# Performance work log

Hardware: AMD Instinct MI355X
Metric: run time of the kernel (lower is better)

The kernel has to match this reference:

```python
import jax, jax.numpy as jnp
import numpy as np
from jax.scipy.linalg import expm

B, Q, F, R, T, H = 2048, 16, 512, 400, 50, 256
STEPS = 100
DT = 1.0 / STEPS
COH = 50.0  # coherence_time


def setup_inputs() -> dict:
    ks = jax.random.split(jax.random.key(0), 48)
    it = iter(range(48))
    def rn(shape, s=1.0):
        return jax.random.normal(ks[next(it)], shape, dtype=jnp.float32) * s
    A = rn((Q, Q)); Bm = rn((Q, Q))
    d = {
        'molecular_features': rn((B, F)),
        'noise': rn((B, T, R), 0.1),          # torch.randn_like * 0.1
        'amp_re': rn((B, Q)), 'amp_im': rn((B, Q)),
        'H_re': (A + A.T) / 2.0,               # hermitized: real part symmetric
        'H_im': (Bm - Bm.T) / 2.0,             # imag part antisymmetric
        'gpc': rn((R,)),
        'bw1': rn((256, Q + F), (Q + F) ** -0.5), 'bb1': rn((256,), 0.01),
        'bw2': rn((128, 256), 256 ** -0.5), 'bb2': rn((128,), 0.01),
        'bw3': rn((R, 128), 128 ** -0.5), 'bb3': rn((R,), 0.01),
    }
    ins = [R, H, H]
    for l in range(3):
        d[f'Wih{l}'] = rn((4 * H, ins[l]), ins[l] ** -0.5)
        d[f'Whh{l}'] = rn((4 * H, H), H ** -0.5)
        d[f'bih{l}'] = rn((4 * H,), 0.01)
        d[f'bhh{l}'] = rn((4 * H,), 0.01)
    d.update({
        'cw1': rn((512, H + R), (H + R) ** -0.5), 'cb1': rn((512,), 0.01),
        'cw2': rn((256, 512), 512 ** -0.5), 'cb2': rn((256,), 0.01),
        'cw3': rn((64, 256), 256 ** -0.5), 'cb3': rn((64,), 0.01),
        'cw4': rn((1, 64), 64 ** -0.5), 'cb4': rn((1,), 0.01),
    })
    return d


def _lstm_layer(x, Wih, Whh, bih, bhh):
    # PyTorch LSTM gate order: i, f, g, o
    def step(carry, xt):
        h, c = carry
        z = xt @ Wih.T + h @ Whh.T + bih + bhh
        ig, fg, gg, og = jnp.split(z, 4, axis=-1)
        c = jax.nn.sigmoid(fg) * c + jax.nn.sigmoid(ig) * jnp.tanh(gg)
        h = jax.nn.sigmoid(og) * jnp.tanh(c)
        return (h, c), h
    n = x.shape[0]
    init = (jnp.zeros((n, H), x.dtype), jnp.zeros((n, H), x.dtype))
    (hT, _), hs = jax.lax.scan(step, init, jnp.swapaxes(x, 0, 1))
    return jnp.swapaxes(hs, 0, 1), hT


def _forward(molecular_features, noise, amp_re, amp_im, H_re, H_im, gpc,
             bw1, bb1, bw2, bb2, bw3, bb3,
             Wih0, Whh0, bih0, bhh0, Wih1, Whh1, bih1, bhh1, Wih2, Whh2, bih2, bhh2,
             cw1, cb1, cw2, cb2, cw3, cb3, cw4, cb4):
    Hp = (H_re + 1j * H_im).astype(jnp.complex64)
    amp = (amp_re + 1j * amp_im).astype(jnp.complex64)
    amp = amp / jnp.linalg.norm(amp, axis=-1, keepdims=True)  # F.normalize
    # molecular interaction Hamiltonian (real part only, as in source)
    M = jnp.einsum('bi,ij->bij', molecular_features[:, :Q], H_re)
    def qstep(a, step):
        t = step * DT
        Ht = Hp[None, :, :] + M * t                 # [B,Q,Q] complex
        U = jax.vmap(expm)(-1j * Ht * DT)           # per-sample matrix_exp
        a = jnp.einsum('bij,bj->bi', U, a) * jnp.exp(-t / COH)
        return a, None
    amp, _ = jax.lax.scan(qstep, amp, jnp.arange(STEPS, dtype=jnp.float32))
    obs = (jnp.abs(amp) ** 2).astype(jnp.float32)   # quantum observables
    bio = jnp.concatenate([obs, molecular_features], axis=-1)  # [B, Q+F]
    h1 = jax.nn.relu(bio @ bw1.T + bb1)
    h2 = jnp.tanh(h1 @ bw2.T + bb2)
    receptor = jax.nn.sigmoid(h2 @ bw3.T + bb3)     # [B, R]
    # biological signal transduction
    g_amp = receptor * jax.nn.sigmoid(gpc)
    adapt = jnp.exp(-jnp.arange(T, dtype=jnp.float32) / 10.0)[None, :, None]
    seq = g_amp[:, None, :] * adapt + noise         # [B, T, R]
    x, hT = _lstm_layer(seq, Wih0, Whh0, bih0, bhh0)
    x, hT = _lstm_layer(x, Wih1, Whh1, bih1, bhh1)
    x, hT = _lstm_layer(x, Wih2, Whh2, bih2, bhh2)  # hT: last-layer hidden [B,H]
    cf = jnp.concatenate([hT, receptor], axis=-1)   # [B, H+R]
    c1 = jax.nn.relu(cf @ cw1.T + cb1)
    c2 = jax.nn.relu(c1 @ cw2.T + cb2)
    c3 = jnp.tanh(c2 @ cw3.T + cb3)
    cons = jnp.mean(jax.nn.sigmoid(c3 @ cw4.T + cb4))
    valence = jnp.mean(jnp.tanh(x), axis=(1, 2))    # [B]
    return receptor, x, valence, cons, amp


def reference(molecular_features, noise, amp_re, amp_im, H_re, H_im, gpc,
              bw1, bb1, bw2, bb2, bw3, bb3,
              Wih0, Whh0, bih0, bhh0, Wih1, Whh1, bih1, bhh1, Wih2, Whh2, bih2, bhh2,
              cw1, cb1, cw2, cb2, cw3, cb3, cw4, cb4):
    receptor, seq, valence, cons, amp = _forward(
        molecular_features, noise, amp_re, amp_im, H_re, H_im, gpc,
        bw1, bb1, bw2, bb2, bw3, bb3,
        Wih0, Whh0, bih0, bhh0, Wih1, Whh1, bih1, bhh1, Wih2, Whh2, bih2, bhh2,
        cw1, cb1, cw2, cb2, cw3, cb3, cw4, cb4)
    # von Neumann entanglement entropy across a 2/2 qubit bipartition (Q=16 -> 4x4)
    half = 2 ** ((int(np.log2(Q))) // 2)
    rs = amp.reshape(amp.shape[0], half, -1)
    rho = jnp.einsum('bij,bik->bjk', rs, jnp.conj(rs))
    ev = jnp.clip(jnp.linalg.eigvals(rho).real, 1e-12, None)
    ent = jnp.mean(-jnp.sum(ev * jnp.log(ev), axis=-1))
    return receptor, seq, valence, cons, ent
```

## Files before the change

### kernel.cpp

```cpp
#include <hip/hip_runtime.h>
#include <stdint.h>


using short8 = __attribute__((ext_vector_type(8))) short;
using f32x4  = __attribute__((ext_vector_type(4))) float;

#define DEV static __device__ __forceinline__

typedef const __attribute__((address_space(1))) void GV;
typedef __attribute__((address_space(3))) void LV;
DEV void gload16(const void* g, void* l) {
  __builtin_amdgcn_global_load_lds((GV*)g, (LV*)l, 16, 0, 0);
}

DEV ushort f2b(float x) {
  union { float f; uint32_t u; } v; v.f = x;
  uint32_t r = v.u + 0x7FFFu + ((v.u >> 16) & 1u);
  return (ushort)(r >> 16);
}
DEV float b2f(ushort x) {
  union { uint32_t u; float f; } v; v.u = ((uint32_t)x) << 16; return v.f;
}
DEV float sigf(float x) { return 1.f / (1.f + __expf(-x)); }
DEV float tanh_fast(float x) {
  float xc = fminf(9.f, fmaxf(-9.f, x));
  float e = __expf(2.f * xc);
  return (e - 1.f) / (e + 1.f);
}

__global__ void k_convw(const float* __restrict__ src, ushort* __restrict__ dst,
                        int sr, int dr, int sc, int dc,
                        const float* __restrict__ scale, int mode) {
  long n = (long)dr * dc;
  for (long idx = (long)blockIdx.x * blockDim.x + threadIdx.x; idx < n;
       idx += (long)gridDim.x * blockDim.x) {
    int r = (int)(idx / dc), c = (int)(idx % dc);
    float v = 0.f;
    if (r < sr && c < sc) {
      v = src[(long)r * sc + c];
      if (mode == 1) v *= sigf(scale[c]);
    }
    dst[idx] = f2b(v);
  }
}

__global__ void k_vadd(const float* __restrict__ a, const float* __restrict__ b,
                       float* __restrict__ o, int n) {
  int i = blockIdx.x * blockDim.x + threadIdx.x;
  if (i < n) o[i] = a[i] + b[i];
}

__global__ __launch_bounds__(128)
void k_quantum(const float* __restrict__ ampr_in, const float* __restrict__ ampi_in,
               const float* __restrict__ Hre, const float* __restrict__ Him,
               const float* __restrict__ mf,
               ushort* __restrict__ bio, float* __restrict__ ampS_r,
               float* __restrict__ ampS_i, int st0) {
  const int gid = blockIdx.x * 128 + threadIdx.x;
  const int b = gid >> 5;
  const int l32 = gid & 31;
  const int i = l32 & 15;
  const int h = l32 >> 4;
  float hre[8], him[8];
#pragma unroll
  for (int jj = 0; jj < 8; jj++) {
    hre[jj] = Hre[i * 16 + h * 8 + jj];
    him[jj] = Him[i * 16 + h * 8 + jj];
  }
  const float mfi = mf[(long)b * 512 + i];
  float are, aim;
  if (st0 == 0) {
    are = ampr_in[b * 16 + i]; aim = ampi_in[b * 16 + i];
    float ss = are * are + aim * aim;
#pragma unroll
    for (int m = 1; m < 32; m <<= 1) ss += __shfl_xor(ss, m, 32);
    ss *= 0.5f;
    const float inv = 1.f / sqrtf(ss);
    are *= inv; aim *= inv;
  } else {
    are = ampS_r[b * 16 + i]; aim = ampS_i[b * 16 + i];
  }
#pragma unroll 1
  for (int st = st0; st < st0 + 25; ++st) {
    const float t = (float)st * 0.01f;
    const float fac = 1.f + t * mfi;
    const float dec = __expf(-t * 0.02f);
    float tre = are, tim = aim, rre = are, rim = aim;
#pragma unroll 1
    for (int k = 1; k <= 6; k++) {
      float w1r = 0.f, w1i = 0.f, w2r = 0.f, w2i = 0.f;
#pragma unroll
      for (int jj = 0; jj < 8; jj++) {
        const float vr = __shfl(tre, h * 8 + jj, 32);
        const float vi = __shfl(tim, h * 8 + jj, 32);
        w1r += hre[jj] * vr; w1i += hre[jj] * vi;
        w2r += him[jj] * vr; w2i += him[jj] * vi;
      }
      w1r += __shfl_xor(w1r, 16, 32);
      w1i += __shfl_xor(w1i, 16, 32);
      w2r += __shfl_xor(w2r, 16, 32);
      w2i += __shfl_xor(w2i, 16, 32);
      const float hr = w1r * fac - w2i;
      const float hi = w1i * fac + w2r;
      const float sk = 0.01f / (float)k;
      tre = sk * hi; tim = -sk * hr;
      rre += tre; rim += tim;
    }
    are = rre * dec; aim = rim * dec;
  }
  if (h == 0) {
    ampS_r[b * 16 + i] = are;
    ampS_i[b * 16 + i] = aim;
    if (bio) bio[(long)b * 576 + i] = f2b(are * are + aim * aim);
  }
}

__global__ void k_biofill(const float* __restrict__ mf, ushort* __restrict__ bio) {
  long i = (long)blockIdx.x * blockDim.x + threadIdx.x;
  if (i < (long)2048 * 512) {
    long b = i >> 9, k = i & 511;
    bio[b * 576 + 16 + k] = f2b(mf[i]);
  }
}

template<int BT>
__global__ __launch_bounds__(256)
void k_gemm(const ushort* __restrict__ A, int lda,
            const ushort* __restrict__ W, int ldw,
            const float* __restrict__ bias,
            const ushort* __restrict__ Gg, int t0,
            float* __restrict__ Cf, int ldcf,
            ushort* __restrict__ Cb, int ldcb,
            int N, int K, int act, int swz) {
  constexpr int FR = BT / 32;
  constexpr int CH = BT / 32;
  __shared__ __align__(16) ushort lsA[2][BT * 64];
  __shared__ __align__(16) ushort lsB[2][BT * 64];
  const int tid = threadIdx.x;
  const int lane = tid & 63, w = tid >> 6;
  const int lr = lane & 15, lq = lane >> 4;
  const int wm = (w >> 1) * (BT / 2), wn = (w & 1) * (BT / 2);
  int bxb = blockIdx.x, byb = blockIdx.y;
  if (swz) {
    const int id = byb * gridDim.x + bxb;
    const int xcd = id & 7, q = id >> 3;
    byb = (q >> 4) * 16 + xcd * 2 + (q & 1);
    bxb = (q >> 1) & 7;
  }
  const int bm = byb * BT, bn = bxb * BT;
  const int srow = lane >> 3;
  const int scol = (((lane & 7) ^ srow)) * 8;

  auto stage = [&](int buf, int kk) {
#pragma unroll
    for (int c = 0; c < CH; c++) {
      const int ch = w * CH + c;
      const int r = ch * 8 + srow;
      gload16(A + (size_t)(bm + r) * lda + kk + scol, lsA[buf] + ch * 512);
      gload16(W + (size_t)(bn + r) * ldw + kk + scol, lsB[buf] + ch * 512);
    }
  };

  f32x4 acc[FR][FR];
#pragma unroll
  for (int i = 0; i < FR; i++)
#pragma unroll
    for (int j = 0; j < FR; j++) acc[i][j] = (f32x4){0.f, 0.f, 0.f, 0.f};

  stage(0, 0);
  __syncthreads();
  const int T = K >> 6;
  for (int t = 0; t < T; t++) {
    const int cur = t & 1;
    if (t + 1 < T) stage(cur ^ 1, (t + 1) * 64);
    short8 af[FR][2], bf[FR][2];
#pragma unroll
    for (int mi = 0; mi < FR; mi++)
#pragma unroll
      for (int k2 = 0; k2 < 2; k2++) {
        const int row = wm + mi * 16 + lr;
        af[mi][k2] = *(const short8*)(lsA[cur] + (row >> 3) * 512 + (row & 7) * 64 +
                                      (((k2 * 4 + lq) ^ (row & 7)) * 8));
      }
#pragma unroll
    for (int ni = 0; ni < FR; ni++)
#pragma unroll
      for (int k2 = 0; k2 < 2; k2++) {
        const int row = wn + ni * 16 + lr;
        bf[ni][k2] = *(const short8*)(lsB[cur] + (row >> 3) * 512 + (row & 7) * 64 +
                                      (((k2 * 4 + lq) ^ (row & 7)) * 8));
      }
#pragma unroll
    for (int k2 = 0; k2 < 2; k2++)
#pragma unroll
      for (int mi = 0; mi < FR; mi++)
#pragma unroll
        for (int ni = 0; ni < FR; ni++)
          acc[mi][ni] = __builtin_amdgcn_mfma_f32_16x16x32_bf16(
              af[mi][k2], bf[ni][k2], acc[mi][ni], 0, 0, 0);
    __syncthreads();
  }

#pragma unroll
  for (int mi = 0; mi < FR; mi++) {
#pragma unroll
    for (int r = 0; r < 4; r++) {
      const int row = bm + wm + mi * 16 + lq * 4 + r;
      float gfac = 0.f; const ushort* ggrow = nullptr;
      if (Gg) {
        gfac = __expf(-(float)(t0 + (row >> 11)) * 0.1f);
        ggrow = Gg + (size_t)(row & 2047) * 1024;
      }
#pragma unroll
      for (int ni = 0; ni < FR; ni++) {
        const int col = bn + wn + ni * 16 + lr;
        if (col < N) {
          float v = acc[mi][ni][r];
          if (bias) v += bias[col];
          if (Gg)  v += gfac * b2f(ggrow[col]);
          if (act == 1) v = fmaxf(v, 0.f);
          else if (act == 2) v = tanh_fast(v);
          else if (act == 3) v = sigf(v);
          if (Cf) Cf[(size_t)row * ldcf + col] = v;
          if (Cb) Cb[(size_t)row * ldcb + col] = f2b(v);
        }
      }
    }
  }
}

__global__ void k_noiseconv(const float* __restrict__ noise, ushort* __restrict__ dst, int t0) {
  long n = 10L * 2048 * 448;
  for (long idx = (long)blockIdx.x * blockDim.x + threadIdx.x; idx < n;
       idx += (long)gridDim.x * blockDim.x) {
    int r = (int)(idx % 448);
    long row = idx / 448;
    int b = (int)(row & 2047);
    int tl = (int)(row >> 11);
    ushort v = 0;
    if (r < 400)
      v = f2b(__builtin_nontemporal_load(&noise[((long)b * 50 + t0 + tl) * 400 + r]));
    dst[idx] = v;
  }
}

__global__ __launch_bounds__(512, 2)
void k_fused(const ushort* __restrict__ IH, const ushort* __restrict__ Whh,
             float* __restrict__ hstate, float* __restrict__ cstate,
             ushort* __restrict__ Hout, float* __restrict__ Xout, int t0,
             const ushort* __restrict__ gA, int glda,
             const ushort* __restrict__ gW,
             const float* __restrict__ gbias, const ushort* __restrict__ gGg,
             int gt0, ushort* __restrict__ gC, int gK) {
  __shared__ __align__(16) ushort upool[37024];
  const int tid = threadIdx.x;

  if (blockIdx.x < 128) {
    ushort (*h_lds)[266] = (ushort(*)[266])upool;
    ushort* ih0 = upool + 4256;
    const int lane = tid & 63, w8 = tid >> 6;
    const int lr = lane & 15, lq = lane >> 4;
    const int b0 = blockIdx.x * 16;
    const int wcols = w8 * 32;

    short8 wres[2][8];
#pragma unroll
    for (int cg = 0; cg < 2; cg++) {
      const ushort* wp = Whh + (size_t)(wcols + cg * 16 + lr) * 256 + lq * 8;
#pragma unroll
      for (int kk = 0; kk < 8; kk++) wres[cg][kk] = *(const short8*)(wp + kk * 32);
    }

    float c_reg[2][4], h_reg[2][4];
#pragma unroll
    for (int cg = 0; cg < 2; cg++) {
      const int j = wcols + cg * 16 + lr;
#pragma unroll
      for (int r = 0; r < 4; r++) {
        const int s = lq * 4 + r;
        float hv = hstate[(size_t)(b0 + s) * 256 + j];
        c_reg[cg][r] = cstate[(size_t)(b0 + s) * 256 + j];
        h_reg[cg][r] = hv;
        h_lds[s][j] = f2b(hv);
      }
    }
    __syncthreads();

#define LOADB(buf, g, cg) { \
  const ushort* wp_ = Whh + (size_t)((g) * 256 + wcols + (cg) * 16 + lr) * 256 + lq * 8; \
  _Pragma("unroll") for (int kk = 0; kk < 8; kk++) (buf)[kk] = *(const short8*)(wp_ + kk * 32); }
#define MFMAB(buf, g, cg) { \
  _Pragma("unroll") for (int kk = 0; kk < 8; kk++) \
    acc[cg][g] = __builtin_amdgcn_mfma_f32_16x16x32_bf16(af[kk], (buf)[kk], acc[cg][g], 0, 0, 0); }
#define MFMAR(cg) { \
  _Pragma("unroll") for (int kk = 0; kk < 8; kk++) \
    acc[cg][0] = __builtin_amdgcn_mfma_f32_16x16x32_bf16(af[kk], wres[cg][kk], acc[cg][0], 0, 0, 0); }

    for (int blk = 0; blk < 10; blk += 2) {
#pragma unroll
      for (int si = 0; si < 2; si++) {
        const ushort* src = IH + ((size_t)(blk + si) * 2048 + b0) * 1024;
#pragma unroll
        for (int u = 0; u < 4; u++) {
          const int bi = u * 8 + w8;
          gload16(src + (size_t)bi * 512 + lane * 8, ih0 + si * 16384 + bi * 512);
        }
      }
      __syncthreads();

      for (int i2 = 0; i2 < 2; i2++) {
        const int tl = blk + i2;
        const ushort* ihc = ih0 + i2 * 16384;
        short8 af[8];
#pragma unroll
        for (int kk = 0; kk < 8; kk++)
          af[kk] = *(const short8*)(&h_lds[lr][kk * 32 + lq * 8]);
        __syncthreads();

        f32x4 acc[2][4];
#pragma unroll
        for (int cg = 0; cg < 2; cg++)
#pragma unroll
          for (int g = 0; g < 4; g++) acc[cg][g] = (f32x4){0.f, 0.f, 0.f, 0.f};

        short8 wb0[8], wb1[8];
        LOADB(wb0, 1, 0);
        LOADB(wb1, 1, 1);
        MFMAR(0);
        MFMAR(1);
        MFMAB(wb0, 1, 0);
        LOADB(wb0, 2, 0);
        MFMAB(wb1, 1, 1);
        LOADB(wb1, 2, 1);
        MFMAB(wb0, 2, 0);
        LOADB(wb0, 3, 0);
        MFMAB(wb1, 2, 1);
        LOADB(wb1, 3, 1);
        MFMAB(wb0, 3, 0);
        MFMAB(wb1, 3, 1);

        const int t = t0 + tl;
#pragma unroll
        for (int cg = 0; cg < 2; cg++) {
          const int j = wcols + cg * 16 + lr;
#pragma unroll
          for (int r = 0; r < 4; r++) {
            const int s = lq * 4 + r;
            const float zi = acc[cg][0][r] + b2f(ihc[s * 1024 + j]);
            const float zf = acc[cg][1][r] + b2f(ihc[s * 1024 + 256 + j]);
            const float zg = acc[cg][2][r] + b2f(ihc[s * 1024 + 512 + j]);
            const float zo = acc[cg][3][r] + b2f(ihc[s * 1024 + 768 + j]);
            const float ig = sigf(zi), fg = sigf(zf), gg = tanh_fast(zg), og = sigf(zo);
            const float c = fg * c_reg[cg][r] + ig * gg;
            c_reg[cg][r] = c;
            const float h = og * tanh_fast(c);
            h_reg[cg][r] = h;
            h_lds[s][j] = f2b(h);
            if (Hout) Hout[((size_t)t * 2048 + b0 + s) * 256 + j] = f2b(h);
            if (Xout)
              __builtin_nontemporal_store(h, &Xout[((size_t)(b0 + s) * 50 + t) * 256 + j]);
          }
        }
        __syncthreads();
      }
    }
#undef LOADB
#undef MFMAB
#undef MFMAR
#pragma unroll
    for (int cg = 0; cg < 2; cg++) {
      const int j = wcols + cg * 16 + lr;
#pragma unroll
      for (int r = 0; r < 4; r++) {
        const int s = lq * 4 + r;
        hstate[(size_t)(b0 + s) * 256 + j] = h_reg[cg][r];
        cstate[(size_t)(b0 + s) * 256 + j] = c_reg[cg][r];
      }
    }
  } else {
    ushort* lsA = upool;
    ushort* lsB = upool + 16384;
    const int gb = blockIdx.x - 128;
    const int xcd = gb & 7, q = gb >> 3;
    const int byb = (q >> 4) * 16 + xcd * 2 + (q & 1);
    const int bxb = (q >> 1) & 7;
    const int bm = byb * 128, bn = bxb * 128;
    const int lane = tid & 63, w4 = tid >> 6;
    const int lr = lane & 15, lq = lane >> 4;
    const int wm = (w4 >> 1) * 64, wn = (w4 & 1) * 64;
    const int srow = lane >> 3;
    const int scol = (((lane & 7) ^ srow)) * 8;
    const bool gact = (tid < 256);

    f32x4 acc[4][4];
#pragma unroll
    for (int i = 0; i < 4; i++)
#pragma unroll
      for (int j = 0; j < 4; j++) acc[i][j] = (f32x4){0.f, 0.f, 0.f, 0.f};

    if (gact) {
#pragma unroll
      for (int c = 0; c < 4; c++) {
        const int ch = w4 * 4 + c;
        const int r = ch * 8 + srow;
        gload16(gA + (size_t)(bm + r) * glda + scol, lsA + ch * 512);
        gload16(gW + (size_t)(bn + r) * glda + scol, lsB + ch * 512);
      }
    }
    __syncthreads();

    const int T = gK >> 6;
    for (int t = 0; t < T; t++) {
      const int cur = t & 1;
      if (gact && t + 1 < T) {
        const int kk = (t + 1) * 64;
#pragma unroll
        for (int c = 0; c < 4; c++) {
          const int ch = w4 * 4 + c;
          const int r = ch * 8 + srow;
          gload16(gA + (size_t)(bm + r) * glda + kk + scol, lsA + (cur ^ 1) * 8192 + ch * 512);
          gload16(gW + (size_t)(bn + r) * glda + kk + scol, lsB + (cur ^ 1) * 8192 + ch * 512);
        }
      }
      if (gact) {
        short8 af[4][2], bf[4][2];
#pragma unroll
        for (int mi = 0; mi < 4; mi++)
#pragma unroll
          for (int k2 = 0; k2 < 2; k2++) {
            const int row = wm + mi * 16 + lr;
            af[mi][k2] = *(const short8*)(lsA + cur * 8192 + (row >> 3) * 512 +
                                          (row & 7) * 64 + (((k2 * 4 + lq) ^ (row & 7)) * 8));
          }
#pragma unroll
        for (int ni = 0; ni < 4; ni++)
#pragma unroll
          for (int k2 = 0; k2 < 2; k2++) {
            const int row = wn + ni * 16 + lr;
            bf[ni][k2] = *(const short8*)(lsB + cur * 8192 + (row >> 3) * 512 +
                                          (row & 7) * 64 + (((k2 * 4 + lq) ^ (row & 7)) * 8));
          }
#pragma unroll
        for (int k2 = 0; k2 < 2; k2++)
#pragma unroll
          for (int mi = 0; mi < 4; mi++)
#pragma unroll
            for (int ni = 0; ni < 4; ni++)
              acc[mi][ni] = __builtin_amdgcn_mfma_f32_16x16x32_bf16(
                  af[mi][k2], bf[ni][k2], acc[mi][ni], 0, 0, 0);
      }
      __syncthreads();
    }

    if (gact) {
#pragma unroll
      for (int mi = 0; mi < 4; mi++) {
#pragma unroll
        for (int r = 0; r < 4; r++) {
          const int row = bm + wm + mi * 16 + lq * 4 + r;
          float gfac = 0.f; const ushort* ggrow = nullptr;
          if (gGg) {
            gfac = __expf(-(float)(gt0 + (row >> 11)) * 0.1f);
            ggrow = gGg + (size_t)(row & 2047) * 1024;
          }
#pragma unroll
          for (int ni = 0; ni < 4; ni++) {
            const int col = bn + wn + ni * 16 + lr;
            float v = acc[mi][ni][r];
            if (gbias) v += gbias[col];
            if (gGg)  v += gfac * b2f(ggrow[col]);
            gC[(size_t)row * 1024 + col] = f2b(v);
          }
        }
      }
    }
  }
}

__global__ void k_cffill(const float* __restrict__ hT, const ushort* __restrict__ recb,
                         ushort* __restrict__ cf) {
  long i = (long)blockIdx.x * blockDim.x + threadIdx.x;
  if (i < (long)2048 * 656) {
    long b = i / 656; int c = (int)(i % 656);
    cf[b * 704 + c] = (c < 256) ? f2b(hT[b * 256 + c]) : recb[b * 448 + (c - 256)];
  }
}

__global__ __launch_bounds__(256)
void k_cons(const float* __restrict__ c3, const float* __restrict__ w4,
            const float* __restrict__ b4, float* __restrict__ out) {
  __shared__ float red[256];
  float accv = 0.f;
  for (int b = threadIdx.x; b < 2048; b += 256) {
    float d = b4[0];
#pragma unroll
    for (int k = 0; k < 64; k++) d += c3[(long)b * 64 + k] * w4[k];
    accv += sigf(d);
  }
  red[threadIdx.x] = accv; __syncthreads();
  for (int s = 128; s > 0; s >>= 1) {
    if (threadIdx.x < s) red[threadIdx.x] += red[threadIdx.x + s];
    __syncthreads();
  }
  if (threadIdx.x == 0) out[0] = red[0] * (1.f / 2048.f);
}

__global__ __launch_bounds__(256)
void k_val(const float* __restrict__ x, float* __restrict__ out) {
  __shared__ float red[256];
  const float* p = x + (size_t)blockIdx.x * 12800;
  float a = 0.f;
  for (int i = threadIdx.x; i < 12800; i += 256) a += tanh_fast(p[i]);
  red[threadIdx.x] = a; __syncthreads();
  for (int s = 128; s > 0; s >>= 1) {
    if (threadIdx.x < s) red[threadIdx.x] += red[threadIdx.x + s];
    __syncthreads();
  }
  if (threadIdx.x == 0) out[blockIdx.x] = red[0] * (1.f / 12800.f);
}

__global__ __launch_bounds__(64)
void k_ent(const float* __restrict__ ar, const float* __restrict__ ai,
           float* __restrict__ partial) {
  __shared__ float red[64];
  const int tid = threadIdx.x;
  const int b = blockIdx.x * 64 + tid;
  float vr[16], vi[16];
#pragma unroll
  for (int i = 0; i < 16; i++) { vr[i] = ar[b * 16 + i]; vi[i] = ai[b * 16 + i]; }
  float m[64];
#pragma unroll
  for (int j = 0; j < 4; j++)
#pragma unroll
    for (int k = 0; k < 4; k++) {
      float re = 0.f, im = 0.f;
#pragma unroll
      for (int i = 0; i < 4; i++) {
        float xr = vr[i * 4 + j], xi = vi[i * 4 + j];
        float yr = vr[i * 4 + k], yi = vi[i * 4 + k];
        re += xr * yr + xi * yi;
        im += xi * yr - xr * yi;
      }
      m[j * 8 + k] = re;
      m[j * 8 + (k + 4)] = -im;
      m[(j + 4) * 8 + k] = im;
      m[(j + 4) * 8 + (k + 4)] = re;
    }
#pragma unroll 1
  for (int sweep = 0; sweep < 6; ++sweep) {
#pragma unroll
    for (int p = 0; p < 7; p++) {
#pragma unroll
      for (int q = p + 1; q < 8; q++) {
        const float apq = m[p * 8 + q];
        if (fabsf(apq) > 1e-28f) {
          const float app = m[p * 8 + p], aqq = m[q * 8 + q];
          const float tau = (aqq - app) / (2.f * apq);
          const float tt = (tau >= 0.f ? 1.f : -1.f) /
                           (fabsf(tau) + sqrtf(1.f + tau * tau));
          const float cc = 1.f / sqrtf(1.f + tt * tt);
          const float ssn = tt * cc;
#pragma unroll
          for (int k2 = 0; k2 < 8; k2++) {
            const float mp = m[p * 8 + k2], mq = m[q * 8 + k2];
            m[p * 8 + k2] = cc * mp - ssn * mq;
            m[q * 8 + k2] = ssn * mp + cc * mq;
          }
#pragma unroll
          for (int k2 = 0; k2 < 8; k2++) {
            const float mp = m[k2 * 8 + p], mq = m[k2 * 8 + q];
            m[k2 * 8 + p] = cc * mp - ssn * mq;
            m[k2 * 8 + q] = ssn * mp + cc * mq;
          }
        }
      }
    }
  }
  float e = 0.f;
#pragma unroll
  for (int k2 = 0; k2 < 8; k2++) {
    const float lam = fmaxf(m[k2 * 8 + k2], 1e-12f);
    e -= lam * logf(lam);
  }
  red[tid] = e; __syncthreads();
  for (int s = 32; s > 0; s >>= 1) {
    if (tid < s) red[tid] += red[tid + s];
    __syncthreads();
  }
  if (tid == 0) partial[blockIdx.x] = red[0];
}

__global__ void k_entfin(const float* __restrict__ partial, float* __restrict__ out) {
  if (threadIdx.x == 0) {
    float s = 0.f;
    for (int i = 0; i < 32; i++) s += partial[i];
    out[0] = s * (0.5f / 2048.f);
  }
}

extern "C" void kernel_launch(void* const* d_in, const int* in_sizes, int n_in,
                              void* d_out, int out_size, void* d_ws, size_t ws_size,
                              hipStream_t stream) {
  (void)in_sizes; (void)n_in; (void)out_size; (void)ws_size;
  const float* mf    = (const float*)d_in[0];
  const float* noise = (const float*)d_in[1];
  const float* ampr  = (const float*)d_in[2];
  const float* ampi  = (const float*)d_in[3];
  const float* Hre   = (const float*)d_in[4];
  const float* Him   = (const float*)d_in[5];
  const float* gpc   = (const float*)d_in[6];
  const float* bw1 = (const float*)d_in[7];  const float* bb1 = (const float*)d_in[8];
  const float* bw2 = (const float*)d_in[9];  const float* bb2 = (const float*)d_in[10];
  const float* bw3 = (const float*)d_in[11]; const float* bb3 = (const float*)d_in[12];
  const float* Wih[3] = {(const float*)d_in[13], (const float*)d_in[17], (const float*)d_in[21]};
  const float* Whh[3] = {(const float*)d_in[14], (const float*)d_in[18], (const float*)d_in[22]};
  const float* bih[3] = {(const float*)d_in[15], (const float*)d_in[19], (const float*)d_in[23]};
  const float* bhh[3] = {(const float*)d_in[16], (const float*)d_in[20], (const float*)d_in[24]};
  const float* cw1 = (const float*)d_in[25]; const float* cb1 = (const float*)d_in[26];
  const float* cw2 = (const float*)d_in[27]; const float* cb2 = (const float*)d_in[28];
  const float* cw3 = (const float*)d_in[29]; const float* cb3 = (const float*)d_in[30];
  const float* cw4 = (const float*)d_in[31]; const float* cb4 = (const float*)d_in[32];

  float* out = (float*)d_out;
  float* out_rec  = out;
  float* out_seq  = out + 819200;
  float* out_val  = out + 27033600;
  float* out_cons = out + 27035648;
  float* out_ent  = out + 27035649;

  char* ws = (char*)d_ws;
  size_t off = 0;
  auto alloc = [&](size_t bytes) -> char* {
    char* p = ws + off; off += (bytes + 255) & ~(size_t)255; return p;
  };
  ushort* WB1   = (ushort*)alloc((size_t)256 * 576 * 2);
  ushort* WB2   = (ushort*)alloc((size_t)128 * 256 * 2);
  ushort* WB3   = (ushort*)alloc((size_t)512 * 128 * 2);
  ushort* WIH0  = (ushort*)alloc((size_t)1024 * 448 * 2);
  ushort* WIH0S = (ushort*)alloc((size_t)1024 * 448 * 2);
  ushort* WIH1  = (ushort*)alloc((size_t)1024 * 256 * 2);
  ushort* WIH2  = (ushort*)alloc((size_t)1024 * 256 * 2);
  ushort* WHH0  = (ushort*)alloc((size_t)1024 * 256 * 2);
  ushort* WHH1  = (ushort*)alloc((size_t)1024 * 256 * 2);
  ushort* WHH2  = (ushort*)alloc((size_t)1024 * 256 * 2);
  ushort* WC1   = (ushort*)alloc((size_t)512 * 704 * 2);
  ushort* WC2   = (ushort*)alloc((size_t)256 * 512 * 2);
  ushort* WC3   = (ushort*)alloc((size_t)128 * 256 * 2);
  float*  BSUM  = (float*)alloc((size_t)3 * 1024 * 4);
  ushort* BIO   = (ushort*)alloc((size_t)2048 * 576 * 2);
  ushort* H1B   = (ushort*)alloc((size_t)2048 * 256 * 2);
  ushort* H2B   = (ushort*)alloc((size_t)2048 * 128 * 2);
  ushort* RECB  = (ushort*)alloc((size_t)2048 * 448 * 2);
  ushort* GGB   = (ushort*)alloc((size_t)2048 * 1024 * 2);
  float*  AMPR  = (float*)alloc((size_t)2048 * 16 * 4);
  float*  AMPI  = (float*)alloc((size_t)2048 * 16 * 4);
  ushort* NCH   = (ushort*)alloc((size_t)10 * 2048 * 448 * 2);
  ushort* IHCA  = (ushort*)alloc((size_t)10 * 2048 * 1024 * 2);
  ushort* IHCB  = (ushort*)alloc((size_t)10 * 2048 * 1024 * 2);
  ushort* HBUF  = (ushort*)alloc((size_t)50 * 2048 * 256 * 2);
  float*  HST   = (float*)alloc((size_t)2048 * 256 * 4);
  float*  CST   = (float*)alloc((size_t)2048 * 256 * 4);
  ushort* CFB   = (ushort*)alloc((size_t)2048 * 704 * 2);
  ushort* C1B   = (ushort*)alloc((size_t)2048 * 512 * 2);
  ushort* C2B   = (ushort*)alloc((size_t)2048 * 256 * 2);
  float*  C3F   = (float*)alloc((size_t)2048 * 64 * 4);
  float*  ENTP  = (float*)alloc((size_t)32 * 4);

  hipMemsetAsync(BIO,  0, (size_t)2048 * 576 * 2, stream);
  hipMemsetAsync(RECB, 0, (size_t)2048 * 448 * 2, stream);
  hipMemsetAsync(CFB,  0, (size_t)2048 * 704 * 2, stream);

  auto convw = [&](const float* src, ushort* dst, int sr, int dr, int sc, int dc,
                   const float* scale, int mode) {
    long n = (long)dr * dc;
    int blocks = (int)((n + 255) / 256); if (blocks > 2048) blocks = 2048;
    hipLaunchKernelGGL(k_convw, dim3(blocks), dim3(256), 0, stream,
                       src, dst, sr, dr, sc, dc, scale, mode);
  };
  convw(bw1, WB1, 256, 256, 528, 576, nullptr, 0);
  convw(bw2, WB2, 128, 128, 256, 256, nullptr, 0);
  convw(bw3, WB3, 400, 512, 128, 128, nullptr, 0);
  convw(Wih[0], WIH0,  1024, 1024, 400, 448, nullptr, 0);
  convw(Wih[0], WIH0S, 1024, 1024, 400, 448, gpc, 1);
  convw(Wih[1], WIH1, 1024, 1024, 256, 256, nullptr, 0);
  convw(Wih[2], WIH2, 1024, 1024, 256, 256, nullptr, 0);
  convw(Whh[0], WHH0, 1024, 1024, 256, 256, nullptr, 0);
  convw(Whh[1], WHH1, 1024, 1024, 256, 256, nullptr, 0);
  convw(Whh[2], WHH2, 1024, 1024, 256, 256, nullptr, 0);
  convw(cw1, WC1, 512, 512, 656, 704, nullptr, 0);
  convw(cw2, WC2, 256, 256, 512, 512, nullptr, 0);
  convw(cw3, WC3,  64, 128, 256, 256, nullptr, 0);
  for (int l = 0; l < 3; l++)
    hipLaunchKernelGGL(k_vadd, dim3(4), dim3(256), 0, stream, bih[l], bhh[l], BSUM + l * 1024, 1024);

  for (int qc = 0; qc < 4; qc++)
    hipLaunchKernelGGL(k_quantum, dim3(512), dim3(128), 0, stream,
                       ampr, ampi, Hre, Him, mf,
                       (qc == 3 ? BIO : (ushort*)nullptr), AMPR, AMPI, qc * 25);
  hipLaunchKernelGGL(k_biofill, dim3(4096), dim3(256), 0, stream, mf, BIO);

  auto gemm = [&](bool big, const ushort* A, int lda, const ushort* W, int ldw,
                  const float* bias, const ushort* Gg, int t0, float* Cf, int ldcf,
                  ushort* Cb, int ldcb, int M, int N, int K, int act) {
    if (big) {
      dim3 grid((N + 127) / 128, M / 128);
      const int swz = (grid.x == 8 && (grid.y & 15) == 0) ? 1 : 0;
      hipLaunchKernelGGL(k_gemm<128>, grid, dim3(256), 0, stream,
                         A, lda, W, ldw, bias, Gg, t0, Cf, ldcf, Cb, ldcb, N, K, act, swz);
    } else {
      dim3 grid((N + 63) / 64, M / 64);
      hipLaunchKernelGGL(k_gemm<64>, grid, dim3(256), 0, stream,
                         A, lda, W, ldw, bias, Gg, t0, Cf, ldcf, Cb, ldcb, N, K, act, 0);
    }
  };

  gemm(false, BIO, 576, WB1, 576, bb1, nullptr, 0, nullptr, 0, H1B, 256, 2048, 256, 576, 1);
  gemm(false, H1B, 256, WB2, 256, bb2, nullptr, 0, nullptr, 0, H2B, 128, 2048, 128, 256, 2);
  gemm(false, H2B, 128, WB3, 128, bb3, nullptr, 0, out_rec, 400, RECB, 448, 2048, 400, 128, 3);
  gemm(false, RECB, 448, WIH0S, 448, nullptr, nullptr, 0, nullptr, 0, GGB, 1024, 2048, 1024, 448, 0);

  const ushort* WHHl[3] = {WHH0, WHH1, WHH2};
  ushort* IHCbuf[2] = {IHCA, IHCB};
  hipLaunchKernelGGL(k_noiseconv, dim3(8192), dim3(256), 0, stream, noise, NCH, 0);
  gemm(true, NCH, 448, WIH0, 448, BSUM, GGB, 0, nullptr, 0, IHCA, 1024, 20480, 1024, 448, 0);

  for (int i = 0; i < 15; i++) {
    const int l = i / 5, c = i % 5;
    if (c == 0) hipMemsetAsync(HST, 0, (size_t)2048 * 256 * 4 * 2, stream);
    const bool hg = (i + 1 < 15);
    const ushort* gA = nullptr; const ushort* gWp = nullptr;
    const float* gb_ = nullptr; const ushort* gGg = nullptr;
    int glda = 256, gK = 256, ggt0 = 0;
    if (hg) {
      const int l2 = (i + 1) / 5, c2 = (i + 1) % 5;
      if (l2 == 0) {
        hipLaunchKernelGGL(k_noiseconv, dim3(8192), dim3(256), 0, stream, noise, NCH, c2 * 10);
        gA = NCH; glda = 448; gK = 448; gb_ = BSUM; gGg = GGB; ggt0 = c2 * 10; gWp = WIH0;
      } else {
        gA = HBUF + (size_t)(c2 * 10) * 2048 * 256; glda = 256; gK = 256;
        gb_ = BSUM + l2 * 1024; gGg = nullptr; ggt0 = 0;
        gWp = (l2 == 1 ? WIH1 : WIH2);
      }
    }
    dim3 grid(hg ? 1408 : 128);
    hipLaunchKernelGGL(k_fused, grid, dim3(512), 0, stream,
                       IHCbuf[i & 1], WHHl[l], HST, CST,
                       (l < 2 ? HBUF : (ushort*)nullptr),
                       (l == 2 ? out_seq : (float*)nullptr), c * 10,
                       gA, glda, gWp, gb_, gGg, ggt0, IHCbuf[(i + 1) & 1], gK);
  }

  hipLaunchKernelGGL(k_cffill, dim3(5256), dim3(256), 0, stream, HST, RECB, CFB);
  gemm(false, CFB, 704, WC1, 704, cb1, nullptr, 0, nullptr, 0, C1B, 512, 2048, 512, 704, 1);
  gemm(false, C1B, 512, WC2, 512, cb2, nullptr, 0, nullptr, 0, C2B, 256, 2048, 256, 512, 1);
  gemm(false, C2B, 256, WC3, 256, cb3, nullptr, 0, C3F, 64, nullptr, 0, 2048, 64, 256, 2);
  hipLaunchKernelGGL(k_cons, dim3(1), dim3(256), 0, stream, C3F, cw4, cb4, out_cons);

  hipLaunchKernelGGL(k_val, dim3(2048), dim3(256), 0, stream, out_seq, out_val);
  hipLaunchKernelGGL(k_ent, dim3(32), dim3(64), 0, stream, AMPR, AMPI, ENTP);
  hipLaunchKernelGGL(k_entfin, dim3(1), dim3(32), 0, stream, ENTP, out_ent);
}
```

Before: 2.833 ms.

## Co-schedule quantum evolution with first input GEMM and fold gate bias into LSTM

Replaces the four chained quantum-evolution launches with one kernel, k_qg. Its first 128 blocks run all 100 steps while the remaining blocks compute the layer-0 input-projection GEMM for the first chunk, so the latency-bound quantum work overlaps with the GEMM. The receptor-dependent gate term (GGB scaled by exp(-0.1t)) moves out of the GEMM epilogue and into the LSTM recurrent kernel, which reads it into registers per block. This removes the dependency of the input GEMM on the receptor MLP chain, but it adds register pressure and per-step expf work inside the recurrent kernel.

```diff
diff --git a/kernel.cpp b/kernel.cpp
--- a/kernel.cpp
+++ b/kernel.cpp
@@ -48,71 +48,6 @@
                        float* __restrict__ o, int n) {
   int i = blockIdx.x * blockDim.x + threadIdx.x;
   if (i < n) o[i] = a[i] + b[i];
-}
-
-__global__ __launch_bounds__(128)
-void k_quantum(const float* __restrict__ ampr_in, const float* __restrict__ ampi_in,
-               const float* __restrict__ Hre, const float* __restrict__ Him,
-               const float* __restrict__ mf,
-               ushort* __restrict__ bio, float* __restrict__ ampS_r,
-               float* __restrict__ ampS_i, int st0) {
-  const int gid = blockIdx.x * 128 + threadIdx.x;
-  const int b = gid >> 5;
-  const int l32 = gid & 31;
-  const int i = l32 & 15;
-  const int h = l32 >> 4;
-  float hre[8], him[8];
-#pragma unroll
-  for (int jj = 0; jj < 8; jj++) {
-    hre[jj] = Hre[i * 16 + h * 8 + jj];
-    him[jj] = Him[i * 16 + h * 8 + jj];
-  }
-  const float mfi = mf[(long)b * 512 + i];
-  float are, aim;
-  if (st0 == 0) {
-    are = ampr_in[b * 16 + i]; aim = ampi_in[b * 16 + i];
-    float ss = are * are + aim * aim;
-#pragma unroll
-    for (int m = 1; m < 32; m <<= 1) ss += __shfl_xor(ss, m, 32);
-    ss *= 0.5f;
-    const float inv = 1.f / sqrtf(ss);
-    are *= inv; aim *= inv;
-  } else {
-    are = ampS_r[b * 16 + i]; aim = ampS_i[b * 16 + i];
-  }
-#pragma unroll 1
-  for (int st = st0; st < st0 + 25; ++st) {
-    const float t = (float)st * 0.01f;
-    const float fac = 1.f + t * mfi;
-    const float dec = __expf(-t * 0.02f);
-    float tre = are, tim = aim, rre = are, rim = aim;
-#pragma unroll 1
-    for (int k = 1; k <= 6; k++) {
-      float w1r = 0.f, w1i = 0.f, w2r = 0.f, w2i = 0.f;
-#pragma unroll
-      for (int jj = 0; jj < 8; jj++) {
-        const float vr = __shfl(tre, h * 8 + jj, 32);
-        const float vi = __shfl(tim, h * 8 + jj, 32);
-        w1r += hre[jj] * vr; w1i += hre[jj] * vi;
-        w2r += him[jj] * vr; w2i += him[jj] * vi;
-      }
-      w1r += __shfl_xor(w1r, 16, 32);
-      w1i += __shfl_xor(w1i, 16, 32);
-      w2r += __shfl_xor(w2r, 16, 32);
-      w2i += __shfl_xor(w2i, 16, 32);
-      const float hr = w1r * fac - w2i;
-      const float hi = w1i * fac + w2r;
-      const float sk = 0.01f / (float)k;
-      tre = sk * hi; tim = -sk * hr;
-      rre += tre; rim += tim;
-    }
-    are = rre * dec; aim = rim * dec;
-  }
-  if (h == 0) {
-    ampS_r[b * 16 + i] = are;
-    ampS_i[b * 16 + i] = aim;
-    if (bio) bio[(long)b * 576 + i] = f2b(are * are + aim * aim);
-  }
 }
 
 __global__ void k_biofill(const float* __restrict__ mf, ushort* __restrict__ bio) {
@@ -245,13 +180,172 @@
 }
 
 __global__ __launch_bounds__(512, 2)
+void k_qg(const float* __restrict__ ampr_in, const float* __restrict__ ampi_in,
+          const float* __restrict__ Hre, const float* __restrict__ Him,
+          const float* __restrict__ mf, ushort* __restrict__ bio,
+          float* __restrict__ ampS_r, float* __restrict__ ampS_i,
+          const ushort* __restrict__ gA, int glda,
+          const ushort* __restrict__ gW, const float* __restrict__ gbias,
+          ushort* __restrict__ gC, int gK) {
+  __shared__ __align__(16) ushort upool[32768];
+  const int tid = threadIdx.x;
+
+  if (blockIdx.x < 128) {
+    const int gid = blockIdx.x * 512 + tid;
+    const int b = gid >> 5;
+    const int l32 = gid & 31;
+    const int i = l32 & 15;
+    const int h = l32 >> 4;
+    float hre[8], him[8];
+#pragma unroll
+    for (int jj = 0; jj < 8; jj++) {
+      hre[jj] = Hre[i * 16 + h * 8 + jj];
+      him[jj] = Him[i * 16 + h * 8 + jj];
+    }
+    const float mfi = mf[(long)b * 512 + i];
+    float are = ampr_in[b * 16 + i], aim = ampi_in[b * 16 + i];
+    float ss = are * are + aim * aim;
+#pragma unroll
+    for (int m = 1; m < 32; m <<= 1) ss += __shfl_xor(ss, m, 32);
+    ss *= 0.5f;
+    const float inv = 1.f / sqrtf(ss);
+    are *= inv; aim *= inv;
+#pragma unroll 1
+    for (int st = 0; st < 100; ++st) {
+      const float t = (float)st * 0.01f;
+      const float fac = 1.f + t * mfi;
+      const float dec = __expf(-t * 0.02f);
+      float tre = are, tim = aim, rre = are, rim = aim;
+#pragma unroll 1
+      for (int k = 1; k <= 6; k++) {
+        float w1r = 0.f, w1i = 0.f, w2r = 0.f, w2i = 0.f;
+#pragma unroll
+        for (int jj = 0; jj < 8; jj++) {
+          const float vr = __shfl(tre, h * 8 + jj, 32);
+          const float vi = __shfl(tim, h * 8 + jj, 32);
+          w1r += hre[jj] * vr; w1i += hre[jj] * vi;
+          w2r += him[jj] * vr; w2i += him[jj] * vi;
+        }
+        w1r += __shfl_xor(w1r, 16, 32);
+        w1i += __shfl_xor(w1i, 16, 32);
+        w2r += __shfl_xor(w2r, 16, 32);
+        w2i += __shfl_xor(w2i, 16, 32);
+        const float hr = w1r * fac - w2i;
+        const float hi = w1i * fac + w2r;
+        const float sk = 0.01f / (float)k;
+        tre = sk * hi; tim = -sk * hr;
+        rre += tre; rim += tim;
+      }
+      are = rre * dec; aim = rim * dec;
+    }
+    if (h == 0) {
+      ampS_r[b * 16 + i] = are;
+      ampS_i[b * 16 + i] = aim;
+      bio[(long)b * 576 + i] = f2b(are * are + aim * aim);
+    }
+  } else {
+    ushort* lsA = upool;
+    ushort* lsB = upool + 16384;
+    const int gb = blockIdx.x - 128;
+    const int xcd = gb & 7, q = gb >> 3;
+    const int byb = (q >> 4) * 16 + xcd * 2 + (q & 1);
+    const int bxb = (q >> 1) & 7;
+    const int bm = byb * 128, bn = bxb * 128;
+    const int lane = tid & 63, w4 = tid >> 6;
+    const int lr = lane & 15, lq = lane >> 4;
+    const int wm = (w4 >> 1) * 64, wn = (w4 & 1) * 64;
+    const int srow = lane >> 3;
+    const int scol = (((lane & 7) ^ srow)) * 8;
+    const bool gact = (tid < 256);
+
+    f32x4 acc[4][4];
+#pragma unroll
+    for (int i = 0; i < 4; i++)
+#pragma unroll
+      for (int j = 0; j < 4; j++) acc[i][j] = (f32x4){0.f, 0.f, 0.f, 0.f};
+
+    if (gact) {
+#pragma unroll
+      for (int c = 0; c < 4; c++) {
+        const int ch = w4 * 4 + c;
+        const int r = ch * 8 + srow;
+        gload16(gA + (size_t)(bm + r) * glda + scol, lsA + ch * 512);
+        gload16(gW + (size_t)(bn + r) * glda + scol, lsB + ch * 512);
+      }
+    }
+    __syncthreads();
+
+    const int T = gK >> 6;
+    for (int t = 0; t < T; t++) {
+      const int cur = t & 1;
+      if (gact && t + 1 < T) {
+        const int kk = (t + 1) * 64;
+#pragma unroll
+        for (int c = 0; c < 4; c++) {
+          const int ch = w4 * 4 + c;
+          const int r = ch * 8 + srow;
+          gload16(gA + (size_t)(bm + r) * glda + kk + scol, lsA + (cur ^ 1) * 8192 + ch * 512);
+          gload16(gW + (size_t)(bn + r) * glda + kk + scol, lsB + (cur ^ 1) * 8192 + ch * 512);
+        }
+      }
+      if (gact) {
+        short8 af[4][2], bf[4][2];
+#pragma unroll
+        for (int mi = 0; mi < 4; mi++)
+#pragma unroll
+          for (int k2 = 0; k2 < 2; k2++) {
+            const int row = wm + mi * 16 + lr;
+            af[mi][k2] = *(const short8*)(lsA + cur * 8192 + (row >> 3) * 512 +
+                                          (row & 7) * 64 + (((k2 * 4 + lq) ^ (row & 7)) * 8));
+          }
+#pragma unroll
+        for (int ni = 0; ni < 4; ni++)
+#pragma unroll
+          for (int k2 = 0; k2 < 2; k2++) {
+            const int row = wn + ni * 16 + lr;
+            bf[ni][k2] = *(const short8*)(lsB + cur * 8192 + (row >> 3) * 512 +
+                                          (row & 7) * 64 + (((k2 * 4 + lq) ^ (row & 7)) * 8));
+          }
+#pragma unroll
+        for (int k2 = 0; k2 < 2; k2++)
+#pragma unroll
+          for (int mi = 0; mi < 4; mi++)
+#pragma unroll
+            for (int ni = 0; ni < 4; ni++)
+              acc[mi][ni] = __builtin_amdgcn_mfma_f32_16x16x32_bf16(
+                  af[mi][k2], bf[ni][k2], acc[mi][ni], 0, 0, 0);
+      }
+      __syncthreads();
+    }
+
+    if (gact) {
+#pragma unroll
+      for (int mi = 0; mi < 4; mi++) {
+#pragma unroll
+        for (int r = 0; r < 4; r++) {
+          const int row = bm + wm + mi * 16 + lq * 4 + r;
+#pragma unroll
+          for (int ni = 0; ni < 4; ni++) {
+            const int col = bn + wn + ni * 16 + lr;
+            float v = acc[mi][ni][r];
+            if (gbias) v += gbias[col];
+            gC[(size_t)row * 1024 + col] = f2b(v);
+          }
+        }
+      }
+    }
+  }
+}
+
+__global__ __launch_bounds__(512, 2)
 void k_fused(const ushort* __restrict__ IH, const ushort* __restrict__ Whh,
+             const ushort* __restrict__ recGg,
              float* __restrict__ hstate, float* __restrict__ cstate,
              ushort* __restrict__ Hout, float* __restrict__ Xout, int t0,
              const ushort* __restrict__ gA, int glda,
              const ushort* __restrict__ gW,
-             const float* __restrict__ gbias, const ushort* __restrict__ gGg,
-             int gt0, ushort* __restrict__ gC, int gK) {
+             const float* __restrict__ gbias,
+             ushort* __restrict__ gC, int gK) {
   __shared__ __align__(16) ushort upool[37024];
   const int tid = threadIdx.x;
 
@@ -270,6 +364,17 @@
 #pragma unroll
       for (int kk = 0; kk < 8; kk++) wres[cg][kk] = *(const short8*)(wp + kk * 32);
     }
+
+    float gg[4][2][4];
+#pragma unroll
+    for (int g = 0; g < 4; g++)
+#pragma unroll
+      for (int cg = 0; cg < 2; cg++)
+#pragma unroll
+        for (int r = 0; r < 4; r++)
+          gg[g][cg][r] = recGg
+              ? b2f(recGg[(size_t)(b0 + lq * 4 + r) * 1024 + g * 256 + wcols + cg * 16 + lr])
+              : 0.f;
 
     float c_reg[2][4], h_reg[2][4];
 #pragma unroll
@@ -340,18 +445,19 @@
         MFMAB(wb1, 3, 1);
 
         const int t = t0 + tl;
+        const float gfac = recGg ? __expf(-(float)t * 0.1f) : 0.f;
 #pragma unroll
         for (int cg = 0; cg < 2; cg++) {
           const int j = wcols + cg * 16 + lr;
 #pragma unroll
           for (int r = 0; r < 4; r++) {
             const int s = lq * 4 + r;
-            const float zi = acc[cg][0][r] + b2f(ihc[s * 1024 + j]);
-            const float zf = acc[cg][1][r] + b2f(ihc[s * 1024 + 256 + j]);
-            const float zg = acc[cg][2][r] + b2f(ihc[s * 1024 + 512 + j]);
-            const float zo = acc[cg][3][r] + b2f(ihc[s * 1024 + 768 + j]);
-            const float ig = sigf(zi), fg = sigf(zf), gg = tanh_fast(zg), og = sigf(zo);
-            const float c = fg * c_reg[cg][r] + ig * gg;
+            const float zi = acc[cg][0][r] + b2f(ihc[s * 1024 + j])       + gfac * gg[0][cg][r];
+            const float zf = acc[cg][1][r] + b2f(ihc[s * 1024 + 256 + j]) + gfac * gg[1][cg][r];
+            const float zg = acc[cg][2][r] + b2f(ihc[s * 1024 + 512 + j]) + gfac * gg[2][cg][r];
+            const float zo = acc[cg][3][r] + b2f(ihc[s * 1024 + 768 + j]) + gfac * gg[3][cg][r];
+            const float ig = sigf(zi), fg = sigf(zf), ggt = tanh_fast(zg), og = sigf(zo);
+            const float c = fg * c_reg[cg][r] + ig * ggt;
             c_reg[cg][r] = c;
             const float h = og * tanh_fast(c);
             h_reg[cg][r] = h;
@@ -458,17 +564,11 @@
 #pragma unroll
         for (int r = 0; r < 4; r++) {
           const int row = bm + wm + mi * 16 + lq * 4 + r;
-          float gfac = 0.f; const ushort* ggrow = nullptr;
-          if (gGg) {
-            gfac = __expf(-(float)(gt0 + (row >> 11)) * 0.1f);
-            ggrow = gGg + (size_t)(row & 2047) * 1024;
-          }
 #pragma unroll
           for (int ni = 0; ni < 4; ni++) {
             const int col = bn + wn + ni * 16 + lr;
             float v = acc[mi][ni][r];
             if (gbias) v += gbias[col];
-            if (gGg)  v += gfac * b2f(ggrow[col]);
             gC[(size_t)row * 1024 + col] = f2b(v);
           }
         }
@@ -693,10 +793,10 @@
   for (int l = 0; l < 3; l++)
     hipLaunchKernelGGL(k_vadd, dim3(4), dim3(256), 0, stream, bih[l], bhh[l], BSUM + l * 1024, 1024);
 
-  for (int qc = 0; qc < 4; qc++)
-    hipLaunchKernelGGL(k_quantum, dim3(512), dim3(128), 0, stream,
-                       ampr, ampi, Hre, Him, mf,
-                       (qc == 3 ? BIO : (ushort*)nullptr), AMPR, AMPI, qc * 25);
+  hipLaunchKernelGGL(k_noiseconv, dim3(8192), dim3(256), 0, stream, noise, NCH, 0);
+  hipLaunchKernelGGL(k_qg, dim3(1408), dim3(512), 0, stream,
+                     ampr, ampi, Hre, Him, mf, BIO, AMPR, AMPI,
+                     NCH, 448, WIH0, BSUM, IHCA, 448);
   hipLaunchKernelGGL(k_biofill, dim3(4096), dim3(256), 0, stream, mf, BIO);
 
   auto gemm = [&](bool big, const ushort* A, int lda, const ushort* W, int ldw,
@@ -721,33 +821,32 @@
 
   const ushort* WHHl[3] = {WHH0, WHH1, WHH2};
   ushort* IHCbuf[2] = {IHCA, IHCB};
-  hipLaunchKernelGGL(k_noiseconv, dim3(8192), dim3(256), 0, stream, noise, NCH, 0);
-  gemm(true, NCH, 448, WIH0, 448, BSUM, GGB, 0, nullptr, 0, IHCA, 1024, 20480, 1024, 448, 0);
 
   for (int i = 0; i < 15; i++) {
     const int l = i / 5, c = i % 5;
     if (c == 0) hipMemsetAsync(HST, 0, (size_t)2048 * 256 * 4 * 2, stream);
     const bool hg = (i + 1 < 15);
     const ushort* gA = nullptr; const ushort* gWp = nullptr;
-    const float* gb_ = nullptr; const ushort* gGg = nullptr;
-    int glda = 256, gK = 256, ggt0 = 0;
+    const float* gb_ = nullptr;
+    int glda = 256, gK = 256;
     if (hg) {
       const int l2 = (i + 1) / 5, c2 = (i + 1) % 5;
       if (l2 == 0) {
         hipLaunchKernelGGL(k_noiseconv, dim3(8192), dim3(256), 0, stream, noise, NCH, c2 * 10);
-        gA = NCH; glda = 448; gK = 448; gb_ = BSUM; gGg = GGB; ggt0 = c2 * 10; gWp = WIH0;
+        gA = NCH; glda = 448; gK = 448; gb_ = BSUM; gWp = WIH0;
       } else {
         gA = HBUF + (size_t)(c2 * 10) * 2048 * 256; glda = 256; gK = 256;
-        gb_ = BSUM + l2 * 1024; gGg = nullptr; ggt0 = 0;
+        gb_ = BSUM + l2 * 1024;
         gWp = (l2 == 1 ? WIH1 : WIH2);
       }
     }
     dim3 grid(hg ? 1408 : 128);
     hipLaunchKernelGGL(k_fused, grid, dim3(512), 0, stream,
-                       IHCbuf[i & 1], WHHl[l], HST, CST,
+                       IHCbuf[i & 1], WHHl[l], (l == 0 ? GGB : (ushort*)nullptr),
+                       HST, CST,
                        (l < 2 ? HBUF : (ushort*)nullptr),
                        (l == 2 ? out_seq : (float*)nullptr), c * 10,
-                       gA, glda, gWp, gb_, gGg, ggt0, IHCbuf[(i + 1) & 1], gK);
+                       gA, glda, gWp, gb_, IHCbuf[(i + 1) & 1], gK);
   }
 
   hipLaunchKernelGGL(k_cffill, dim3(5256), dim3(256), 0, stream, HST, RECB, CFB);
```

Measured after the change: 3.683 ms. +30.0%, slower.
